# Optimization experiments

Hardware: AMD Instinct MI355X
Metric: run time of the kernel (lower is better)

The kernel has to match this reference:

```python
import jax, jax.numpy as jnp
import numpy as np

N_NODES = 100000
N_EDGES = 1600000
N_GRAPHS = 256
EPS = 1e-5  # GraphNorm / BatchNorm eps


def _seg_sum(x, seg, n):
    return jax.ops.segment_sum(x, seg, num_segments=n)


def setup_inputs() -> dict:
    key = jax.random.key(0)
    ks = jax.random.split(key, 24)
    f32 = jnp.float32

    def nrm(k, shape, s=0.05):
        return jax.random.normal(k, shape, f32) * s

    inp = {}
    inp["x"] = jax.random.normal(ks[0], (N_NODES, 64), f32)
    inp["edge_attr"] = jax.random.normal(ks[1], (N_EDGES, 8), f32)
    # edge_mlp: Linear(8,16) -> ReLU -> Linear(16,1); final bias +2 keeps degrees positive
    inp["em_w1"] = nrm(ks[2], (16, 8), 0.1); inp["em_b1"] = jnp.zeros((16,), f32)
    inp["em_w2"] = nrm(ks[3], (1, 16), 0.1); inp["em_b2"] = jnp.full((1,), 2.0, f32)
    # GCNConv weights stored (in, out); PyG GCNConv lin has no bias, separate bias after aggregation
    inp["conv_w0"] = nrm(ks[4], (64, 128)); inp["conv_b0"] = jnp.zeros((128,), f32)
    inp["conv_w1"] = nrm(ks[5], (128, 128)); inp["conv_b1"] = jnp.zeros((128,), f32)
    inp["conv_w2"] = nrm(ks[6], (128, 128)); inp["conv_b2"] = jnp.zeros((128,), f32)
    # GraphNorm params: weight=1, bias=0, mean_scale=1 (PyG init)
    for i in range(3):
        inp[f"gn_w{i}"] = jnp.ones((128,), f32)
        inp[f"gn_b{i}"] = jnp.zeros((128,), f32)
        inp[f"gn_ms{i}"] = jnp.ones((128,), f32)
    # MLP head (weights stored (in,out)); BatchNorm1d eval: running_mean=0, running_var=1
    inp["lin_w0"] = nrm(ks[7], (128, 256)); inp["lin_b0"] = jnp.zeros((256,), f32)
    inp["bn_g0"] = jnp.ones((256,), f32); inp["bn_b0"] = jnp.zeros((256,), f32)
    inp["lin_w1"] = nrm(ks[8], (256, 128)); inp["lin_b1"] = jnp.zeros((128,), f32)
    inp["bn_g1"] = jnp.ones((128,), f32); inp["bn_b1"] = jnp.zeros((128,), f32)
    inp["out_w"] = nrm(ks[9], (128, 1)); inp["out_b"] = jnp.zeros((1,), f32)
    inp["edge_index"] = jax.random.randint(ks[10], (2, N_EDGES), 0, N_NODES)
    inp["batch"] = jnp.sort(jax.random.randint(ks[11], (N_NODES,), 0, N_GRAPHS))
    return inp


def _gcn_conv(h, W, b, src, tgt, ew):
    # PyG GCNConv with edge_weight: add self-loops (weight 1), symmetric normalization
    hw = h @ W  # [N, out]
    deg = _seg_sum(ew, tgt, N_NODES) + 1.0  # in-degree incl. self-loop
    dinv = jnp.where(deg > 0, jax.lax.rsqrt(deg), 0.0)
    norm_e = dinv[src] * ew * dinv[tgt]  # [E]
    agg = _seg_sum(norm_e[:, None] * hw[src], tgt, N_NODES)
    agg = agg + (dinv * dinv)[:, None] * hw  # self-loop contribution
    return agg + b


def _graph_norm(h, batch, w, b, ms, cnt):
    mean = _seg_sum(h, batch, N_GRAPHS) / cnt[:, None]  # [G, C]
    sub = h - ms * mean[batch]
    var = _seg_sum(sub * sub, batch, N_GRAPHS) / cnt[:, None]
    return w * sub / jnp.sqrt(var + EPS)[batch] + b


def reference(x, edge_attr, em_w1, em_b1, em_w2, em_b2,
              conv_w0, conv_b0, conv_w1, conv_b1, conv_w2, conv_b2,
              gn_w0, gn_b0, gn_ms0, gn_w1, gn_b1, gn_ms1, gn_w2, gn_b2, gn_ms2,
              lin_w0, lin_b0, bn_g0, bn_b0, lin_w1, lin_b1, bn_g1, bn_b1,
              out_w, out_b, edge_index, batch):
    src, tgt = edge_index[0], edge_index[1]
    ew = (jax.nn.relu(edge_attr @ em_w1.T + em_b1) @ em_w2.T + em_b2).reshape(-1)  # [E]
    cnt = jnp.maximum(_seg_sum(jnp.ones((N_NODES,), x.dtype), batch, N_GRAPHS), 1.0)

    h = x
    layers = [(conv_w0, conv_b0, gn_w0, gn_b0, gn_ms0),
              (conv_w1, conv_b1, gn_w1, gn_b1, gn_ms1),
              (conv_w2, conv_b2, gn_w2, gn_b2, gn_ms2)]
    for W, b, gw, gb, gms in layers:
        h = _gcn_conv(h, W, b, src, tgt, ew)
        h = _graph_norm(h, batch, gw, gb, gms, cnt)
        h = jax.nn.relu(h)  # dropout is identity in eval mode

    pooled = _seg_sum(h, batch, N_GRAPHS) / cnt[:, None]  # global_mean_pool [G, 128]

    inv = 1.0 / jnp.sqrt(1.0 + EPS)  # BatchNorm1d eval: mean=0, var=1
    h = jax.nn.relu((pooled @ lin_w0 + lin_b0) * inv * bn_g0 + bn_b0)
    h = jax.nn.relu((h @ lin_w1 + lin_b1) * inv * bn_g1 + bn_b1)
    out = h @ out_w + out_b  # [G, 1]
    return (out, h)
```

## Files before the change

kernel.cpp:

```cpp
#include <hip/hip_runtime.h>

#define N_NODES 100000
#define N_EDGES 1600000
#define N_GRAPHS 256
#define EPS 1e-5f

#define SCAN_BLOCKS ((N_NODES + 255) / 256)

#define EB 6250
#define CB 3125
#define WB 128
#define W0B 32
#define PREP_BLOCKS (EB + CB + WB + W0B + 2)

typedef __attribute__((ext_vector_type(8))) short bfrag8;
typedef __attribute__((ext_vector_type(4))) float facc4;

__device__ __forceinline__ void fma4(float4& a, float s, const float4& w) {
  a.x += s * w.x; a.y += s * w.y; a.z += s * w.z; a.w += s * w.w;
}

__device__ __forceinline__ unsigned short f2bf(float f) {
  union { float f; unsigned u; } x;
  x.f = f;
  unsigned r = x.u + 0x7FFF + ((x.u >> 16) & 1);
  return (unsigned short)(r >> 16);
}
__device__ __forceinline__ unsigned packbf(float a, float b) {
  return (unsigned)f2bf(a) | ((unsigned)f2bf(b) << 16);
}
__device__ __forceinline__ float4 bf4(unsigned lo, unsigned hi) {
  union { unsigned u; float f; } a, b, c, d;
  a.u = lo << 16;
  b.u = lo & 0xFFFF0000u;
  c.u = hi << 16;
  d.u = hi & 0xFFFF0000u;
  return make_float4(a.f, b.f, c.f, d.f);
}
__device__ __forceinline__ float bfat(const unsigned* tb, int idx) {
  unsigned u = tb[idx >> 1];
  union { unsigned u; float f; } v;
  v.u = (idx & 1) ? (u & 0xFFFF0000u) : (u << 16);
  return v.f;
}

__global__ __launch_bounds__(256) void k_prep(
    const float* __restrict__ ea, const float* __restrict__ w1,
    const float* __restrict__ b1, const float* __restrict__ w2,
    const float* __restrict__ b2, const int* __restrict__ tgt,
    float* __restrict__ ew, int* __restrict__ rowcnt, int* __restrict__ rank,
    const float* __restrict__ x, unsigned* __restrict__ xb,
    const float* __restrict__ cw1, const float* __restrict__ cw2,
    unsigned short* __restrict__ wt1, unsigned short* __restrict__ wt2,
    const float* __restrict__ cw0, unsigned short* __restrict__ wt0,
    const int* __restrict__ batch, int* __restrict__ start) {
  __shared__ float W1[128], B1[16], W2[16];
  const int b = blockIdx.x;
  const int t = threadIdx.x;
  if (b < EB) {
    if (t < 128) W1[t] = w1[t];
    if (t < 16) { B1[t] = b1[t]; W2[t] = w2[t]; }
    __syncthreads();
    int e = b * 256 + t;
    if (e >= N_EDGES) return;
    const float4* ap = (const float4*)(ea + (size_t)e * 8);
    float4 a0 = ap[0], a1 = ap[1];
    float a[8] = {a0.x, a0.y, a0.z, a0.w, a1.x, a1.y, a1.z, a1.w};
    float out = b2[0];
#pragma unroll
    for (int i = 0; i < 16; ++i) {
      float h = B1[i];
#pragma unroll
      for (int j = 0; j < 8; ++j) h += a[j] * W1[i * 8 + j];
      out += fmaxf(h, 0.f) * W2[i];
    }
    ew[e] = out;
    rank[e] = atomicAdd(&rowcnt[tgt[e]], 1);
  } else if (b < EB + CB) {
    int i = (b - EB) * 256 + t;
    if (i >= N_NODES * 64 / 8) return;
    const float4* p = (const float4*)(x + (size_t)i * 8);
    float4 a = p[0], bb = p[1];
    uint4 o;
    o.x = packbf(a.x, a.y);
    o.y = packbf(a.z, a.w);
    o.z = packbf(bb.x, bb.y);
    o.w = packbf(bb.z, bb.w);
    ((uint4*)xb)[i] = o;
  } else if (b < EB + CB + WB) {
    int lb = b - EB - CB;
    int half = lb >> 6;
    int id = (lb & 63) * 256 + t;
    const float* w = half ? cw2 : cw1;
    unsigned short* o = half ? wt2 : wt1;
    int n = id >> 7, k = id & 127;
    o[n * 128 + k] = f2bf(w[k * 128 + n]);
  } else if (b < EB + CB + WB + W0B) {
    int id = (b - EB - CB - WB) * 256 + t;
    if (id >= 8192) return;
    int n = id >> 6, k = id & 63;
    wt0[n * 64 + k] = f2bf(cw0[k * 128 + n]);
  } else {
    int g = (b - EB - CB - WB - W0B) * 256 + t;
    if (g > N_GRAPHS) return;
    int lo = 0, hi = N_NODES;
    while (lo < hi) {
      int mid = (lo + hi) >> 1;
      if (batch[mid] < g) lo = mid + 1; else hi = mid;
    }
    start[g] = lo;
  }
}

__global__ __launch_bounds__(256) void k_scan1(const int* __restrict__ cnt,
                                               int* __restrict__ bsum) {
  int i = blockIdx.x * 256 + threadIdx.x;
  int v = (i < N_NODES) ? cnt[i] : 0;
#pragma unroll
  for (int off = 32; off; off >>= 1) v += __shfl_down(v, off);
  __shared__ int ws[4];
  if ((threadIdx.x & 63) == 0) ws[threadIdx.x >> 6] = v;
  __syncthreads();
  if (threadIdx.x == 0) bsum[blockIdx.x] = ws[0] + ws[1] + ws[2] + ws[3];
}

__global__ __launch_bounds__(512) void k_scan2(const int* __restrict__ bsum,
                                               int* __restrict__ boff) {
  __shared__ int s[512];
  int t = threadIdx.x;
  s[t] = (t < SCAN_BLOCKS) ? bsum[t] : 0;
  __syncthreads();
  for (int off = 1; off < 512; off <<= 1) {
    int u = (t >= off) ? s[t - off] : 0;
    __syncthreads();
    s[t] += u;
    __syncthreads();
  }
  boff[t] = (t == 0) ? 0 : s[t - 1];
}

__global__ __launch_bounds__(256) void k_scan3(const int* __restrict__ cnt,
                                               const int* __restrict__ boff,
                                               int* __restrict__ rowstart) {
  __shared__ int s[256];
  int t = threadIdx.x;
  int i = blockIdx.x * 256 + t;
  int v = (i < N_NODES) ? cnt[i] : 0;
  s[t] = v;
  __syncthreads();
  for (int off = 1; off < 256; off <<= 1) {
    int u = (t >= off) ? s[t - off] : 0;
    __syncthreads();
    s[t] += u;
    __syncthreads();
  }
  if (i < N_NODES) {
    int pre = boff[blockIdx.x] + s[t] - v;
    rowstart[i] = pre;
    if (i == N_NODES - 1) rowstart[N_NODES] = pre + v;
  }
}

__global__ __launch_bounds__(256) void k_fill(
    const int* __restrict__ src, const int* __restrict__ tgt,
    const float* __restrict__ ew, const int* __restrict__ rank,
    const int* __restrict__ rowstart, uint2* __restrict__ meta) {
  int e = blockIdx.x * 256 + threadIdx.x;
  if (e >= N_EDGES) return;
  int p = rowstart[tgt[e]] + rank[e];
  union { float f; unsigned u; } w;
  w.f = ew[e];
  meta[p] = make_uint2(w.u, (unsigned)src[e]);
}

__global__ __launch_bounds__(256) void k_deg(const uint2* __restrict__ meta,
                                             const int* __restrict__ rowstart,
                                             float* __restrict__ dinv) {
  int n = blockIdx.x * 256 + threadIdx.x;
  if (n >= N_NODES) return;
  int rs = rowstart[n], re = rowstart[n + 1];
  float d = 1.f;
  for (int j = rs; j < re; ++j) {
    union { unsigned u; float f; } w;
    w.u = meta[j].x;
    d += w.f;
  }
  dinv[n] = d > 0.f ? rsqrtf(d) : 0.f;
}

__global__ __launch_bounds__(256) void k_scale(uint2* __restrict__ meta,
                                               const int* __restrict__ rowstart,
                                               const float* __restrict__ dinv) {
  int n = blockIdx.x * 4 + (threadIdx.x >> 6);
  if (n >= N_NODES) return;
  int lane = threadIdx.x & 63;
  int rs = rowstart[n], re = rowstart[n + 1];
  float dv = dinv[n];
  for (int j = rs + lane; j < re; j += 64) {
    uint2 m = meta[j];
    union { unsigned u; float f; } w;
    w.u = m.x;
    w.f *= dinv[m.y] * dv;
    meta[j].x = w.u;
  }
}

__global__ __launch_bounds__(256) void k_gather64b(
    const unsigned* __restrict__ xb, const uint2* __restrict__ meta,
    const int* __restrict__ rowstart, const float* __restrict__ dinv,
    unsigned* __restrict__ aggxb) {
  const int t = threadIdx.x;
  const int n = blockIdx.x * 4 + (t >> 6);
  if (n >= N_NODES) return;
  const unsigned lane = t & 63;
  const unsigned q = lane >> 4;
  const unsigned cl = lane & 15;
  const int rs = rowstart[n], re = rowstart[n + 1];
  const uint2* x2 = (const uint2*)xb;
  float4 a0 = make_float4(0.f, 0.f, 0.f, 0.f);
  float4 a1 = make_float4(0.f, 0.f, 0.f, 0.f);
  int j = rs;
  for (; j + 8 <= re; j += 8) {
    uint2 m0 = meta[j + q], m1 = meta[j + 4 + q];
    union { unsigned u; float f; } w0, w1;
    w0.u = m0.x; w1.u = m1.x;
    uint2 v0 = x2[(m0.y << 4) + cl];
    uint2 v1 = x2[(m1.y << 4) + cl];
    fma4(a0, w0.f, bf4(v0.x, v0.y));
    fma4(a1, w1.f, bf4(v1.x, v1.y));
  }
  for (; j + 4 <= re; j += 4) {
    uint2 m0 = meta[j + q];
    union { unsigned u; float f; } w0;
    w0.u = m0.x;
    uint2 v0 = x2[(m0.y << 4) + cl];
    fma4(a0, w0.f, bf4(v0.x, v0.y));
  }
  if (j + (int)q < re) {
    uint2 m0 = meta[j + q];
    union { unsigned u; float f; } w0;
    w0.u = m0.x;
    uint2 v0 = x2[(m0.y << 4) + cl];
    fma4(a1, w0.f, bf4(v0.x, v0.y));
  }
  a0.x += a1.x; a0.y += a1.y; a0.z += a1.z; a0.w += a1.w;
#pragma unroll
  for (int m = 16; m <= 32; m <<= 1) {
    a0.x += __shfl_xor(a0.x, m);
    a0.y += __shfl_xor(a0.y, m);
    a0.z += __shfl_xor(a0.z, m);
    a0.w += __shfl_xor(a0.w, m);
  }
  if (q == 0) {
    float dv = dinv[n];
    uint2 hvb = x2[((unsigned)n << 4) + cl];
    float4 hv = bf4(hvb.x, hvb.y);
    uint2 o;
    o.x = packbf(a0.x + dv * dv * hv.x, a0.y + dv * dv * hv.y);
    o.y = packbf(a0.z + dv * dv * hv.z, a0.w + dv * dv * hv.w);
    *(uint2*)&aggxb[(size_t)n * 32 + cl * 2] = o;
  }
}

__global__ __launch_bounds__(256) void k_hw_mfma0(
    const unsigned short* __restrict__ aggxb,
    const unsigned short* __restrict__ wt0, const float* __restrict__ bias,
    unsigned short* __restrict__ h1b) {
  __shared__ unsigned short Asb[64][72];
  __shared__ unsigned short Wsb[128][72];
  const int t = threadIdx.x;
  const int base = blockIdx.x * 64;

  for (int i = t; i < 1024; i += 256) {
    int nr = i >> 3, k8 = (i & 7) * 8;
    *(uint4*)&Wsb[nr][k8] = *(const uint4*)&wt0[nr * 64 + k8];
  }
  {
    const int ln = t >> 2;
    const int kp = (t & 3) * 16;
    const int n = base + ln;
    if (n < N_NODES) {
      *(uint4*)&Asb[ln][kp] = *(const uint4*)&aggxb[(size_t)n * 64 + kp];
      *(uint4*)&Asb[ln][kp + 8] = *(const uint4*)&aggxb[(size_t)n * 64 + kp + 8];
    } else {
      uint4 z = make_uint4(0, 0, 0, 0);
      *(uint4*)&Asb[ln][kp] = z;
      *(uint4*)&Asb[ln][kp + 8] = z;
    }
  }
  __syncthreads();

  const int wv = t >> 6;
  const int lr = t & 15;
  const int lk = (t >> 4) & 3;
  const int m0 = wv * 16;

  bfrag8 af[2];
#pragma unroll
  for (int kc = 0; kc < 2; ++kc)
    af[kc] = *(const bfrag8*)&Asb[m0 + lr][kc * 32 + lk * 8];

#pragma unroll
  for (int nt = 0; nt < 8; ++nt) {
    facc4 c = {0.f, 0.f, 0.f, 0.f};
#pragma unroll
    for (int kc = 0; kc < 2; ++kc) {
      bfrag8 bf = *(const bfrag8*)&Wsb[nt * 16 + lr][kc * 32 + lk * 8];
      c = __builtin_amdgcn_mfma_f32_16x16x32_bf16(af[kc], bf, c, 0, 0, 0);
    }
    int col = nt * 16 + lr;
    float bv = bias[col];
#pragma unroll
    for (int r = 0; r < 4; ++r) {
      int n = base + m0 + lk * 4 + r;
      if (n < N_NODES) h1b[(size_t)n * 128 + col] = f2bf(c[r] + bv);
    }
  }
}

__global__ __launch_bounds__(256) void k_hw_mfma(
    const unsigned* __restrict__ hb, const unsigned short* __restrict__ wt,
    const int* __restrict__ batch, const float* __restrict__ An,
    const float* __restrict__ Bn, unsigned short* __restrict__ hwb) {
  __shared__ unsigned short Asb[64][136];
  __shared__ unsigned short Wsb[128][136];
  const int t = threadIdx.x;
  const int base = blockIdx.x * 64;

  for (int i = t; i < 2048; i += 256) {
    int nr = i >> 4, k8 = (i & 15) * 8;
    *(uint4*)&Wsb[nr][k8] = *(const uint4*)&wt[nr * 128 + k8];
  }
  {
    const int ln = t >> 2;
    const int cg = (t & 3) * 32;
    const int n = base + ln;
    if (n < N_NODES) {
      const int g = batch[n];
      const uint4* hp = (const uint4*)(hb + (size_t)n * 64);
      const float* Ap = An + (size_t)g * 128;
      const float* Bp = Bn + (size_t)g * 128;
#pragma unroll
      for (int qq = 0; qq < 4; ++qq) {
        int c = cg + qq * 8;
        uint4 v = hp[(t & 3) * 4 + qq];
        float4 lo = bf4(v.x, v.y);
        float4 hi = bf4(v.z, v.w);
        float4 Alo = *(const float4*)&Ap[c], Blo = *(const float4*)&Bp[c];
        float4 Ahi = *(const float4*)&Ap[c + 4], Bhi = *(const float4*)&Bp[c + 4];
        uint4 o;
        o.x = packbf(fmaxf(Alo.x * lo.x + Blo.x, 0.f),
                     fmaxf(Alo.y * lo.y + Blo.y, 0.f));
        o.y = packbf(fmaxf(Alo.z * lo.z + Blo.z, 0.f),
                     fmaxf(Alo.w * lo.w + Blo.w, 0.f));
        o.z = packbf(fmaxf(Ahi.x * hi.x + Bhi.x, 0.f),
                     fmaxf(Ahi.y * hi.y + Bhi.y, 0.f));
        o.w = packbf(fmaxf(Ahi.z * hi.z + Bhi.z, 0.f),
                     fmaxf(Ahi.w * hi.w + Bhi.w, 0.f));
        *(uint4*)&Asb[ln][c] = o;
      }
    } else {
      uint4 z = make_uint4(0, 0, 0, 0);
#pragma unroll
      for (int qq = 0; qq < 4; ++qq) *(uint4*)&Asb[ln][cg + qq * 8] = z;
    }
  }
  __syncthreads();

  const int wv = t >> 6;
  const int lr = t & 15;
  const int lk = (t >> 4) & 3;
  const int m0 = wv * 16;

  bfrag8 af[4];
#pragma unroll
  for (int kc = 0; kc < 4; ++kc)
    af[kc] = *(const bfrag8*)&Asb[m0 + lr][kc * 32 + lk * 8];

#pragma unroll
  for (int nt = 0; nt < 8; ++nt) {
    facc4 c = {0.f, 0.f, 0.f, 0.f};
#pragma unroll
    for (int kc = 0; kc < 4; ++kc) {
      bfrag8 bf = *(const bfrag8*)&Wsb[nt * 16 + lr][kc * 32 + lk * 8];
      c = __builtin_amdgcn_mfma_f32_16x16x32_bf16(af[kc], bf, c, 0, 0, 0);
    }
    int col = nt * 16 + lr;
#pragma unroll
    for (int r = 0; r < 4; ++r) {
      int n = base + m0 + lk * 4 + r;
      if (n < N_NODES) hwb[(size_t)n * 128 + col] = f2bf(c[r]);
    }
  }
}

__global__ __launch_bounds__(256) void k_gatherb(
    const unsigned* __restrict__ hwb, const uint2* __restrict__ meta,
    const int* __restrict__ rowstart, const float* __restrict__ dinv,
    const float* __restrict__ bias, unsigned* __restrict__ aggb) {
  const int t = threadIdx.x;
  const int n = blockIdx.x * 4 + (t >> 6);
  if (n >= N_NODES) return;
  const unsigned lane = t & 63;
  const unsigned q = lane >> 5;
  const unsigned cl = lane & 31;
  const int rs = rowstart[n], re = rowstart[n + 1];
  const uint2* hb = (const uint2*)hwb;
  float4 a0 = make_float4(0.f, 0.f, 0.f, 0.f);
  float4 a1 = make_float4(0.f, 0.f, 0.f, 0.f);
  float4 a2 = make_float4(0.f, 0.f, 0.f, 0.f);
  float4 a3 = make_float4(0.f, 0.f, 0.f, 0.f);
  int j = rs;
  for (; j + 8 <= re; j += 8) {
    uint2 m0 = meta[j + q], m1 = meta[j + 2 + q];
    uint2 m2 = meta[j + 4 + q], m3 = meta[j + 6 + q];
    union { unsigned u; float f; } w0, w1, w2, w3;
    w0.u = m0.x; w1.u = m1.x; w2.u = m2.x; w3.u = m3.x;
    uint2 v0 = hb[(m0.y << 5) + cl];
    uint2 v1 = hb[(m1.y << 5) + cl];
    uint2 v2 = hb[(m2.y << 5) + cl];
    uint2 v3 = hb[(m3.y << 5) + cl];
    fma4(a0, w0.f, bf4(v0.x, v0.y));
    fma4(a1, w1.f, bf4(v1.x, v1.y));
    fma4(a2, w2.f, bf4(v2.x, v2.y));
    fma4(a3, w3.f, bf4(v3.x, v3.y));
  }
  for (; j + 4 <= re; j += 4) {
    uint2 m0 = meta[j + q], m1 = meta[j + 2 + q];
    union { unsigned u; float f; } w0, w1;
    w0.u = m0.x; w1.u = m1.x;
    uint2 v0 = hb[(m0.y << 5) + cl];
    uint2 v1 = hb[(m1.y << 5) + cl];
    fma4(a0, w0.f, bf4(v0.x, v0.y));
    fma4(a1, w1.f, bf4(v1.x, v1.y));
  }
  for (; j + 2 <= re; j += 2) {
    uint2 m0 = meta[j + q];
    union { unsigned u; float f; } w0;
    w0.u = m0.x;
    uint2 v0 = hb[(m0.y << 5) + cl];
    fma4(a0, w0.f, bf4(v0.x, v0.y));
  }
  if (q == 0 && j < re) {
    uint2 m0 = meta[j];
    union { unsigned u; float f; } w0;
    w0.u = m0.x;
    uint2 v0 = hb[(m0.y << 5) + cl];
    fma4(a1, w0.f, bf4(v0.x, v0.y));
  }
  a0.x += a1.x + a2.x + a3.x;
  a0.y += a1.y + a2.y + a3.y;
  a0.z += a1.z + a2.z + a3.z;
  a0.w += a1.w + a2.w + a3.w;
  a0.x += __shfl_xor(a0.x, 32);
  a0.y += __shfl_xor(a0.y, 32);
  a0.z += __shfl_xor(a0.z, 32);
  a0.w += __shfl_xor(a0.w, 32);
  if (q == 0) {
    float dv = dinv[n];
    uint2 hvb = hb[((unsigned)n << 5) + cl];
    float4 hv = bf4(hvb.x, hvb.y);
    float4 bv = ((const float4*)bias)[cl];
    uint2 o;
    o.x = packbf(a0.x + dv * dv * hv.x + bv.x, a0.y + dv * dv * hv.y + bv.y);
    o.y = packbf(a0.z + dv * dv * hv.z + bv.z, a0.w + dv * dv * hv.w + bv.w);
    *(uint2*)&aggb[(size_t)n * 64 + cl * 2] = o;
  }
}

__global__ __launch_bounds__(512) void k_gstats(
    const unsigned* __restrict__ hb, const int* __restrict__ start,
    const float* __restrict__ gw, const float* __restrict__ gb,
    const float* __restrict__ gms, float* __restrict__ An,
    float* __restrict__ Bn) {
  int g = blockIdx.x;
  int s = start[g], e = start[g + 1];
  int t = threadIdx.x, p = t >> 7, c = t & 127;
  float sum = 0.f, sq = 0.f;
  for (int n = s + p; n < e; n += 4) {
    float v = bfat(hb + (size_t)n * 64, c);
    sum += v;
    sq += v * v;
  }
  __shared__ float S[4][128], Q[4][128];
  S[p][c] = sum;
  Q[p][c] = sq;
  __syncthreads();
  if (t < 128) {
    float cnt = (float)max(e - s, 1);
    float mean = (S[0][t] + S[1][t] + S[2][t] + S[3][t]) / cnt;
    float e2 = (Q[0][t] + Q[1][t] + Q[2][t] + Q[3][t]) / cnt;
    float ms = gms[t];
    float var = fmaxf(e2 - ms * (2.f - ms) * mean * mean, 0.f);
    float scale = gw[t] / sqrtf(var + EPS);
    An[(size_t)g * 128 + t] = scale;
    Bn[(size_t)g * 128 + t] = gb[t] - scale * ms * mean;
  }
}

__global__ __launch_bounds__(512) void k_pool(
    const unsigned* __restrict__ hb, const int* __restrict__ start,
    const float* __restrict__ An, const float* __restrict__ Bn,
    float* __restrict__ pooled) {
  int g = blockIdx.x;
  int s = start[g], e = start[g + 1];
  int t = threadIdx.x, p = t >> 7, c = t & 127;
  float A = An[(size_t)g * 128 + c], B = Bn[(size_t)g * 128 + c];
  float sum = 0.f;
  for (int n = s + p; n < e; n += 4)
    sum += fmaxf(A * bfat(hb + (size_t)n * 64, c) + B, 0.f);
  __shared__ float S[4][128];
  S[p][c] = sum;
  __syncthreads();
  if (t < 128) {
    float cnt = (float)max(e - s, 1);
    pooled[g * 128 + t] = (S[0][t] + S[1][t] + S[2][t] + S[3][t]) / cnt;
  }
}

__global__ __launch_bounds__(256) void k_head(
    const float* __restrict__ pooled, const float* __restrict__ w0,
    const float* __restrict__ b0, const float* __restrict__ g0,
    const float* __restrict__ bb0, const float* __restrict__ w1,
    const float* __restrict__ b1, const float* __restrict__ g1,
    const float* __restrict__ bb1, const float* __restrict__ ow,
    const float* __restrict__ ob, float* __restrict__ out) {
  __shared__ float p[128], h1[256], h2[128];
  int g = blockIdx.x, t = threadIdx.x;
  const float inv = 1.0f / sqrtf(1.0f + EPS);
  if (t < 128) p[t] = pooled[g * 128 + t];
  __syncthreads();
  {
    float acc = b0[t];
#pragma unroll 8
    for (int k = 0; k < 128; ++k) acc += p[k] * w0[k * 256 + t];
    h1[t] = fmaxf(acc * inv * g0[t] + bb0[t], 0.f);
  }
  __syncthreads();
  if (t < 128) {
    float acc = b1[t];
#pragma unroll 8
    for (int k = 0; k < 256; ++k) acc += h1[k] * w1[k * 128 + t];
    float v = fmaxf(acc * inv * g1[t] + bb1[t], 0.f);
    h2[t] = v;
    out[N_GRAPHS + g * 128 + t] = v;
  }
  __syncthreads();
  if (t < 64) {
    float v = h2[t] * ow[t] + h2[t + 64] * ow[t + 64];
#pragma unroll
    for (int off = 32; off; off >>= 1) v += __shfl_down(v, off);
    if (t == 0) out[g] = v + ob[0];
  }
}

extern "C" void kernel_launch(void* const* d_in, const int* in_sizes, int n_in,
                              void* d_out, int out_size, void* d_ws,
                              size_t ws_size, hipStream_t stream) {
  const float* x = (const float*)d_in[0];
  const float* edge_attr = (const float*)d_in[1];
  const float* em_w1 = (const float*)d_in[2];
  const float* em_b1 = (const float*)d_in[3];
  const float* em_w2 = (const float*)d_in[4];
  const float* em_b2 = (const float*)d_in[5];
  const float* conv_w[3] = {(const float*)d_in[6], (const float*)d_in[8],
                            (const float*)d_in[10]};
  const float* conv_b[3] = {(const float*)d_in[7], (const float*)d_in[9],
                            (const float*)d_in[11]};
  const float* gn_w[3] = {(const float*)d_in[12], (const float*)d_in[15],
                          (const float*)d_in[18]};
  const float* gn_b[3] = {(const float*)d_in[13], (const float*)d_in[16],
                          (const float*)d_in[19]};
  const float* gn_ms[3] = {(const float*)d_in[14], (const float*)d_in[17],
                           (const float*)d_in[20]};
  const float* lin_w0 = (const float*)d_in[21];
  const float* lin_b0 = (const float*)d_in[22];
  const float* bn_g0 = (const float*)d_in[23];
  const float* bn_b0 = (const float*)d_in[24];
  const float* lin_w1 = (const float*)d_in[25];
  const float* lin_b1 = (const float*)d_in[26];
  const float* bn_g1 = (const float*)d_in[27];
  const float* bn_b1 = (const float*)d_in[28];
  const float* out_w = (const float*)d_in[29];
  const float* out_b = (const float*)d_in[30];
  const int* edge_index = (const int*)d_in[31];
  const int* batch = (const int*)d_in[32];
  const int* src = edge_index;
  const int* tgt = edge_index + N_EDGES;

  char* w = (char*)d_ws;
  size_t off = 0;
  auto carve = [&](size_t bytes) {
    void* p = w + off;
    off = (off + bytes + 511) & ~(size_t)511;
    return p;
  };
  float* ew = (float*)carve((size_t)N_EDGES * 4);
  int* rank = (int*)carve((size_t)N_EDGES * 4);
  float* dinv = (float*)carve((size_t)N_NODES * 4);
  int* rowcnt = (int*)carve((size_t)N_NODES * 4);
  int* rowstart = (int*)carve((size_t)(N_NODES + 1) * 4);
  int* bsum = (int*)carve((size_t)SCAN_BLOCKS * 4);
  int* boff = (int*)carve((size_t)512 * 4);
  uint2* meta = (uint2*)carve((size_t)N_EDGES * 8);
  int* start = (int*)carve((N_GRAPHS + 1) * 4);
  float* AB = (float*)carve((size_t)6 * N_GRAPHS * 128 * 4);
  unsigned* xb = (unsigned*)carve((size_t)N_NODES * 64 * 2);
  unsigned* aggxb = (unsigned*)carve((size_t)N_NODES * 64 * 2);
  unsigned* h1b = (unsigned*)carve((size_t)N_NODES * 128 * 2);
  unsigned* hwb = (unsigned*)carve((size_t)N_NODES * 128 * 2);
  unsigned* agg1b = (unsigned*)carve((size_t)N_NODES * 128 * 2);
  unsigned* agg2b = (unsigned*)carve((size_t)N_NODES * 128 * 2);
  unsigned short* wt0 = (unsigned short*)carve((size_t)128 * 64 * 2);
  unsigned short* wt1 = (unsigned short*)carve((size_t)128 * 128 * 2);
  unsigned short* wt2 = (unsigned short*)carve((size_t)128 * 128 * 2);
  float* pooled = (float*)carve((size_t)N_GRAPHS * 128 * 4);

  float* A0 = AB, *B0 = AB + N_GRAPHS * 128;
  float* A1 = AB + 2 * N_GRAPHS * 128, *B1 = AB + 3 * N_GRAPHS * 128;
  float* A2 = AB + 4 * N_GRAPHS * 128, *B2 = AB + 5 * N_GRAPHS * 128;

  hipMemsetAsync(rowcnt, 0, (size_t)N_NODES * 4, stream);

  k_prep<<<PREP_BLOCKS, 256, 0, stream>>>(
      edge_attr, em_w1, em_b1, em_w2, em_b2, tgt, ew, rowcnt, rank, x, xb,
      conv_w[1], conv_w[2], wt1, wt2, conv_w[0], wt0, batch, start);
  k_scan1<<<SCAN_BLOCKS, 256, 0, stream>>>(rowcnt, bsum);
  k_scan2<<<1, 512, 0, stream>>>(bsum, boff);
  k_scan3<<<SCAN_BLOCKS, 256, 0, stream>>>(rowcnt, boff, rowstart);
  k_fill<<<(N_EDGES + 255) / 256, 256, 0, stream>>>(src, tgt, ew, rank,
                                                    rowstart, meta);
  k_deg<<<(N_NODES + 255) / 256, 256, 0, stream>>>(meta, rowstart, dinv);
  k_scale<<<(N_NODES + 3) / 4, 256, 0, stream>>>(meta, rowstart, dinv);

  const int ggrid = (N_NODES + 3) / 4;
  const int hwgrid = (N_NODES + 63) / 64;

  k_gather64b<<<ggrid, 256, 0, stream>>>(xb, meta, rowstart, dinv, aggxb);
  k_hw_mfma0<<<hwgrid, 256, 0, stream>>>((unsigned short*)aggxb, wt0,
                                         conv_b[0], (unsigned short*)h1b);
  k_gstats<<<N_GRAPHS, 512, 0, stream>>>(h1b, start, gn_w[0], gn_b[0],
                                         gn_ms[0], A0, B0);
  k_hw_mfma<<<hwgrid, 256, 0, stream>>>(h1b, wt1, batch, A0, B0,
                                        (unsigned short*)hwb);
  k_gatherb<<<ggrid, 256, 0, stream>>>(hwb, meta, rowstart, dinv, conv_b[1],
                                       agg1b);
  k_gstats<<<N_GRAPHS, 512, 0, stream>>>(agg1b, start, gn_w[1], gn_b[1],
                                         gn_ms[1], A1, B1);
  k_hw_mfma<<<hwgrid, 256, 0, stream>>>(agg1b, wt2, batch, A1, B1,
                                        (unsigned short*)hwb);
  k_gatherb<<<ggrid, 256, 0, stream>>>(hwb, meta, rowstart, dinv, conv_b[2],
                                       agg2b);
  k_gstats<<<N_GRAPHS, 512, 0, stream>>>(agg2b, start, gn_w[2], gn_b[2],
                                         gn_ms[2], A2, B2);

  k_pool<<<N_GRAPHS, 512, 0, stream>>>(agg2b, start, A2, B2, pooled);
  k_head<<<N_GRAPHS, 256, 0, stream>>>(pooled, lin_w0, lin_b0, bn_g0, bn_b0,
                                       lin_w1, lin_b1, bn_g1, bn_b1, out_w,
                                       out_b, (float*)d_out);
}
```

Before: 520.3 us.

## Fold source-side degree normalization into features and widen gather loads

Symmetric GCN normalization is refactored: the source-side dinv factor is folded into the feature rows (at x->bf16 conversion and in the MFMA epilogue), and the target-side factor is applied once after aggregation, so edge weights no longer need a separate per-edge rescale pass. The deg and scale kernels are merged into one wave-per-node kernel that also does the x conversion, removing a pass over meta. The gather kernels switch to 16-byte loads with fewer lanes per row. Rounding changes slightly because dinv is applied before the bf16 cast.

Measured after the change: 525.5 us. Within noise of the previous version (+1.0%).

```diff
diff --git a/kernel.cpp b/kernel.cpp
--- a/kernel.cpp
+++ b/kernel.cpp
@@ -8,10 +8,9 @@
 #define SCAN_BLOCKS ((N_NODES + 255) / 256)
 
 #define EB 6250
-#define CB 3125
 #define WB 128
 #define W0B 32
-#define PREP_BLOCKS (EB + CB + WB + W0B + 2)
+#define PREP_BLOCKS (EB + WB + W0B + 2)
 
 typedef __attribute__((ext_vector_type(8))) short bfrag8;
 typedef __attribute__((ext_vector_type(4))) float facc4;
@@ -49,7 +48,6 @@
     const float* __restrict__ b1, const float* __restrict__ w2,
     const float* __restrict__ b2, const int* __restrict__ tgt,
     float* __restrict__ ew, int* __restrict__ rowcnt, int* __restrict__ rank,
-    const float* __restrict__ x, unsigned* __restrict__ xb,
     const float* __restrict__ cw1, const float* __restrict__ cw2,
     unsigned short* __restrict__ wt1, unsigned short* __restrict__ wt2,
     const float* __restrict__ cw0, unsigned short* __restrict__ wt0,
@@ -76,32 +74,21 @@
     }
     ew[e] = out;
     rank[e] = atomicAdd(&rowcnt[tgt[e]], 1);
-  } else if (b < EB + CB) {
-    int i = (b - EB) * 256 + t;
-    if (i >= N_NODES * 64 / 8) return;
-    const float4* p = (const float4*)(x + (size_t)i * 8);
-    float4 a = p[0], bb = p[1];
-    uint4 o;
-    o.x = packbf(a.x, a.y);
-    o.y = packbf(a.z, a.w);
-    o.z = packbf(bb.x, bb.y);
-    o.w = packbf(bb.z, bb.w);
-    ((uint4*)xb)[i] = o;
-  } else if (b < EB + CB + WB) {
-    int lb = b - EB - CB;
+  } else if (b < EB + WB) {
+    int lb = b - EB;
     int half = lb >> 6;
     int id = (lb & 63) * 256 + t;
     const float* w = half ? cw2 : cw1;
     unsigned short* o = half ? wt2 : wt1;
     int n = id >> 7, k = id & 127;
     o[n * 128 + k] = f2bf(w[k * 128 + n]);
-  } else if (b < EB + CB + WB + W0B) {
-    int id = (b - EB - CB - WB) * 256 + t;
+  } else if (b < EB + WB + W0B) {
+    int id = (b - EB - WB) * 256 + t;
     if (id >= 8192) return;
     int n = id >> 6, k = id & 63;
     wt0[n * 64 + k] = f2bf(cw0[k * 128 + n]);
   } else {
-    int g = (b - EB - CB - WB - W0B) * 256 + t;
+    int g = (b - EB - WB - W0B) * 256 + t;
     if (g > N_GRAPHS) return;
     int lo = 0, hi = N_NODES;
     while (lo < hi) {
@@ -173,35 +160,28 @@
   meta[p] = make_uint2(w.u, (unsigned)src[e]);
 }
 
-__global__ __launch_bounds__(256) void k_deg(const uint2* __restrict__ meta,
-                                             const int* __restrict__ rowstart,
-                                             float* __restrict__ dinv) {
-  int n = blockIdx.x * 256 + threadIdx.x;
+__global__ __launch_bounds__(256) void k_degcvt(
+    const uint2* __restrict__ meta, const int* __restrict__ rowstart,
+    const float* __restrict__ x, float* __restrict__ dinv,
+    unsigned* __restrict__ xb) {
+  const int n = blockIdx.x * 4 + (threadIdx.x >> 6);
   if (n >= N_NODES) return;
-  int rs = rowstart[n], re = rowstart[n + 1];
-  float d = 1.f;
-  for (int j = rs; j < re; ++j) {
+  const int lane = threadIdx.x & 63;
+  const int rs = rowstart[n], re = rowstart[n + 1];
+  float s = 0.f;
+  for (int j = rs + lane; j < re; j += 64) {
     union { unsigned u; float f; } w;
     w.u = meta[j].x;
-    d += w.f;
-  }
-  dinv[n] = d > 0.f ? rsqrtf(d) : 0.f;
-}
-
-__global__ __launch_bounds__(256) void k_scale(uint2* __restrict__ meta,
-                                               const int* __restrict__ rowstart,
-                                               const float* __restrict__ dinv) {
-  int n = blockIdx.x * 4 + (threadIdx.x >> 6);
-  if (n >= N_NODES) return;
-  int lane = threadIdx.x & 63;
-  int rs = rowstart[n], re = rowstart[n + 1];
-  float dv = dinv[n];
-  for (int j = rs + lane; j < re; j += 64) {
-    uint2 m = meta[j];
-    union { unsigned u; float f; } w;
-    w.u = m.x;
-    w.f *= dinv[m.y] * dv;
-    meta[j].x = w.u;
+    s += w.f;
+  }
+#pragma unroll
+  for (int m = 1; m < 64; m <<= 1) s += __shfl_xor(s, m);
+  float d = 1.f + s;
+  float dv = d > 0.f ? rsqrtf(d) : 0.f;
+  if (lane == 0) dinv[n] = dv;
+  if (lane < 32) {
+    float2 v = ((const float2*)x)[(size_t)n * 32 + lane];
+    xb[((unsigned)n << 5) + lane] = packbf(dv * v.x, dv * v.y);
   }
 }
 
@@ -213,52 +193,63 @@
   const int n = blockIdx.x * 4 + (t >> 6);
   if (n >= N_NODES) return;
   const unsigned lane = t & 63;
-  const unsigned q = lane >> 4;
-  const unsigned cl = lane & 15;
+  const unsigned q = lane >> 3;
+  const unsigned cl = lane & 7;
   const int rs = rowstart[n], re = rowstart[n + 1];
-  const uint2* x2 = (const uint2*)xb;
-  float4 a0 = make_float4(0.f, 0.f, 0.f, 0.f);
-  float4 a1 = make_float4(0.f, 0.f, 0.f, 0.f);
+  const uint4* x4 = (const uint4*)xb;
+  float4 lo0 = make_float4(0.f, 0.f, 0.f, 0.f), hi0 = lo0;
+  float4 lo1 = lo0, hi1 = lo0;
   int j = rs;
-  for (; j + 8 <= re; j += 8) {
-    uint2 m0 = meta[j + q], m1 = meta[j + 4 + q];
+  for (; j + 16 <= re; j += 16) {
+    uint2 m0 = meta[j + q], m1 = meta[j + 8 + q];
     union { unsigned u; float f; } w0, w1;
     w0.u = m0.x; w1.u = m1.x;
-    uint2 v0 = x2[(m0.y << 4) + cl];
-    uint2 v1 = x2[(m1.y << 4) + cl];
-    fma4(a0, w0.f, bf4(v0.x, v0.y));
-    fma4(a1, w1.f, bf4(v1.x, v1.y));
-  }
-  for (; j + 4 <= re; j += 4) {
+    uint4 v0 = x4[(m0.y << 3) + cl];
+    uint4 v1 = x4[(m1.y << 3) + cl];
+    fma4(lo0, w0.f, bf4(v0.x, v0.y));
+    fma4(hi0, w0.f, bf4(v0.z, v0.w));
+    fma4(lo1, w1.f, bf4(v1.x, v1.y));
+    fma4(hi1, w1.f, bf4(v1.z, v1.w));
+  }
+  for (; j + 8 <= re; j += 8) {
     uint2 m0 = meta[j + q];
     union { unsigned u; float f; } w0;
     w0.u = m0.x;
-    uint2 v0 = x2[(m0.y << 4) + cl];
-    fma4(a0, w0.f, bf4(v0.x, v0.y));
+    uint4 v0 = x4[(m0.y << 3) + cl];
+    fma4(lo0, w0.f, bf4(v0.x, v0.y));
+    fma4(hi0, w0.f, bf4(v0.z, v0.w));
   }
   if (j + (int)q < re) {
     uint2 m0 = meta[j + q];
     union { unsigned u; float f; } w0;
     w0.u = m0.x;
-    uint2 v0 = x2[(m0.y << 4) + cl];
-    fma4(a1, w0.f, bf4(v0.x, v0.y));
-  }
-  a0.x += a1.x; a0.y += a1.y; a0.z += a1.z; a0.w += a1.w;
-#pragma unroll
-  for (int m = 16; m <= 32; m <<= 1) {
-    a0.x += __shfl_xor(a0.x, m);
-    a0.y += __shfl_xor(a0.y, m);
-    a0.z += __shfl_xor(a0.z, m);
-    a0.w += __shfl_xor(a0.w, m);
+    uint4 v0 = x4[(m0.y << 3) + cl];
+    fma4(lo1, w0.f, bf4(v0.x, v0.y));
+    fma4(hi1, w0.f, bf4(v0.z, v0.w));
+  }
+  lo0.x += lo1.x; lo0.y += lo1.y; lo0.z += lo1.z; lo0.w += lo1.w;
+  hi0.x += hi1.x; hi0.y += hi1.y; hi0.z += hi1.z; hi0.w += hi1.w;
+#pragma unroll
+  for (int m = 8; m <= 32; m <<= 1) {
+    lo0.x += __shfl_xor(lo0.x, m);
+    lo0.y += __shfl_xor(lo0.y, m);
+    lo0.z += __shfl_xor(lo0.z, m);
+    lo0.w += __shfl_xor(lo0.w, m);
+    hi0.x += __shfl_xor(hi0.x, m);
+    hi0.y += __shfl_xor(hi0.y, m);
+    hi0.z += __shfl_xor(hi0.z, m);
+    hi0.w += __shfl_xor(hi0.w, m);
   }
   if (q == 0) {
     float dv = dinv[n];
-    uint2 hvb = x2[((unsigned)n << 4) + cl];
-    float4 hv = bf4(hvb.x, hvb.y);
-    uint2 o;
-    o.x = packbf(a0.x + dv * dv * hv.x, a0.y + dv * dv * hv.y);
-    o.y = packbf(a0.z + dv * dv * hv.z, a0.w + dv * dv * hv.w);
-    *(uint2*)&aggxb[(size_t)n * 32 + cl * 2] = o;
+    uint4 sv = x4[((unsigned)n << 3) + cl];
+    float4 slo = bf4(sv.x, sv.y), shi = bf4(sv.z, sv.w);
+    uint4 o;
+    o.x = packbf(dv * (lo0.x + slo.x), dv * (lo0.y + slo.y));
+    o.y = packbf(dv * (lo0.z + slo.z), dv * (lo0.w + slo.w));
+    o.z = packbf(dv * (hi0.x + shi.x), dv * (hi0.y + shi.y));
+    o.w = packbf(dv * (hi0.z + shi.z), dv * (hi0.w + shi.w));
+    ((uint4*)aggxb)[((unsigned)n << 3) + cl] = o;
   }
 }
 
@@ -321,7 +312,8 @@
 __global__ __launch_bounds__(256) void k_hw_mfma(
     const unsigned* __restrict__ hb, const unsigned short* __restrict__ wt,
     const int* __restrict__ batch, const float* __restrict__ An,
-    const float* __restrict__ Bn, unsigned short* __restrict__ hwb) {
+    const float* __restrict__ Bn, const float* __restrict__ dinv,
+    unsigned short* __restrict__ hwb) {
   __shared__ unsigned short Asb[64][136];
   __shared__ unsigned short Wsb[128][136];
   const int t = threadIdx.x;
@@ -377,6 +369,13 @@
   for (int kc = 0; kc < 4; ++kc)
     af[kc] = *(const bfrag8*)&Asb[m0 + lr][kc * 32 + lk * 8];
 
+  float dv[4];
+#pragma unroll
+  for (int r = 0; r < 4; ++r) {
+    int n = base + m0 + lk * 4 + r;
+    dv[r] = (n < N_NODES) ? dinv[n] : 0.f;
+  }
+
 #pragma unroll
   for (int nt = 0; nt < 8; ++nt) {
     facc4 c = {0.f, 0.f, 0.f, 0.f};
@@ -389,7 +388,7 @@
 #pragma unroll
     for (int r = 0; r < 4; ++r) {
       int n = base + m0 + lk * 4 + r;
-      if (n < N_NODES) hwb[(size_t)n * 128 + col] = f2bf(c[r]);
+      if (n < N_NODES) hwb[(size_t)n * 128 + col] = f2bf(dv[r] * c[r]);
     }
   }
 }
@@ -402,69 +401,65 @@
   const int n = blockIdx.x * 4 + (t >> 6);
   if (n >= N_NODES) return;
   const unsigned lane = t & 63;
-  const unsigned q = lane >> 5;
-  const unsigned cl = lane & 31;
+  const unsigned q = lane >> 4;
+  const unsigned cl = lane & 15;
   const int rs = rowstart[n], re = rowstart[n + 1];
-  const uint2* hb = (const uint2*)hwb;
-  float4 a0 = make_float4(0.f, 0.f, 0.f, 0.f);
-  float4 a1 = make_float4(0.f, 0.f, 0.f, 0.f);
-  float4 a2 = make_float4(0.f, 0.f, 0.f, 0.f);
-  float4 a3 = make_float4(0.f, 0.f, 0.f, 0.f);
+  const uint4* hb4 = (const uint4*)hwb;
+  float4 lo0 = make_float4(0.f, 0.f, 0.f, 0.f), hi0 = lo0;
+  float4 lo1 = lo0, hi1 = lo0;
   int j = rs;
   for (; j + 8 <= re; j += 8) {
-    uint2 m0 = meta[j + q], m1 = meta[j + 2 + q];
-    uint2 m2 = meta[j + 4 + q], m3 = meta[j + 6 + q];
-    union { unsigned u; float f; } w0, w1, w2, w3;
-    w0.u = m0.x; w1.u = m1.x; w2.u = m2.x; w3.u = m3.x;
-    uint2 v0 = hb[(m0.y << 5) + cl];
-    uint2 v1 = hb[(m1.y << 5) + cl];
-    uint2 v2 = hb[(m2.y << 5) + cl];
-    uint2 v3 = hb[(m3.y << 5) + cl];
-    fma4(a0, w0.f, bf4(v0.x, v0.y));
-    fma4(a1, w1.f, bf4(v1.x, v1.y));
-    fma4(a2, w2.f, bf4(v2.x, v2.y));
-    fma4(a3, w3.f, bf4(v3.x, v3.y));
-  }
-  for (; j + 4 <= re; j += 4) {
-    uint2 m0 = meta[j + q], m1 = meta[j + 2 + q];
+    uint2 m0 = meta[j + q], m1 = meta[j + 4 + q];
     union { unsigned u; float f; } w0, w1;
     w0.u = m0.x; w1.u = m1.x;
-    uint2 v0 = hb[(m0.y << 5) + cl];
-    uint2 v1 = hb[(m1.y << 5) + cl];
-    fma4(a0, w0.f, bf4(v0.x, v0.y));
-    fma4(a1, w1.f, bf4(v1.x, v1.y));
-  }
-  for (; j + 2 <= re; j += 2) {
+    uint4 v0 = hb4[(m0.y << 4) + cl];
+    uint4 v1 = hb4[(m1.y << 4) + cl];
+    fma4(lo0, w0.f, bf4(v0.x, v0.y));
+    fma4(hi0, w0.f, bf4(v0.z, v0.w));
+    fma4(lo1, w1.f, bf4(v1.x, v1.y));
+    fma4(hi1, w1.f, bf4(v1.z, v1.w));
+  }
+  for (; j + 4 <= re; j += 4) {
     uint2 m0 = meta[j + q];
     union { unsigned u; float f; } w0;
     w0.u = m0.x;
-    uint2 v0 = hb[(m0.y << 5) + cl];
-    fma4(a0, w0.f, bf4(v0.x, v0.y));
-  }
-  if (q == 0 && j < re) {
-    uint2 m0 = meta[j];
+    uint4 v0 = hb4[(m0.y << 4) + cl];
+    fma4(lo0, w0.f, bf4(v0.x, v0.y));
+    fma4(hi0, w0.f, bf4(v0.z, v0.w));
+  }
+  if (j + (int)q < re) {
+    uint2 m0 = meta[j + q];
     union { unsigned u; float f; } w0;
     w0.u = m0.x;
-    uint2 v0 = hb[(m0.y << 5) + cl];
-    fma4(a1, w0.f, bf4(v0.x, v0.y));
-  }
-  a0.x += a1.x + a2.x + a3.x;
-  a0.y += a1.y + a2.y + a3.y;
-  a0.z += a1.z + a2.z + a3.z;
-  a0.w += a1.w + a2.w + a3.w;
-  a0.x += __shfl_xor(a0.x, 32);
-  a0.y += __shfl_xor(a0.y, 32);
-  a0.z += __shfl_xor(a0.z, 32);
-  a0.w += __shfl_xor(a0.w, 32);
+    uint4 v0 = hb4[(m0.y << 4) + cl];
+    fma4(lo1, w0.f, bf4(v0.x, v0.y));
+    fma4(hi1, w0.f, bf4(v0.z, v0.w));
+  }
+  lo0.x += lo1.x; lo0.y += lo1.y; lo0.z += lo1.z; lo0.w += lo1.w;
+  hi0.x += hi1.x; hi0.y += hi1.y; hi0.z += hi1.z; hi0.w += hi1.w;
+#pragma unroll
+  for (int m = 16; m <= 32; m <<= 1) {
+    lo0.x += __shfl_xor(lo0.x, m);
+    lo0.y += __shfl_xor(lo0.y, m);
+    lo0.z += __shfl_xor(lo0.z, m);
+    lo0.w += __shfl_xor(lo0.w, m);
+    hi0.x += __shfl_xor(hi0.x, m);
+    hi0.y += __shfl_xor(hi0.y, m);
+    hi0.z += __shfl_xor(hi0.z, m);
+    hi0.w += __shfl_xor(hi0.w, m);
+  }
   if (q == 0) {
     float dv = dinv[n];
-    uint2 hvb = hb[((unsigned)n << 5) + cl];
-    float4 hv = bf4(hvb.x, hvb.y);
-    float4 bv = ((const float4*)bias)[cl];
-    uint2 o;
-    o.x = packbf(a0.x + dv * dv * hv.x + bv.x, a0.y + dv * dv * hv.y + bv.y);
-    o.y = packbf(a0.z + dv * dv * hv.z + bv.z, a0.w + dv * dv * hv.w + bv.w);
-    *(uint2*)&aggb[(size_t)n * 64 + cl * 2] = o;
+    uint4 sv = hb4[((unsigned)n << 4) + cl];
+    float4 slo = bf4(sv.x, sv.y), shi = bf4(sv.z, sv.w);
+    float4 blo = *(const float4*)&bias[cl * 8];
+    float4 bhi = *(const float4*)&bias[cl * 8 + 4];
+    uint4 o;
+    o.x = packbf(dv * (lo0.x + slo.x) + blo.x, dv * (lo0.y + slo.y) + blo.y);
+    o.y = packbf(dv * (lo0.z + slo.z) + blo.z, dv * (lo0.w + slo.w) + blo.w);
+    o.z = packbf(dv * (hi0.x + shi.x) + bhi.x, dv * (hi0.y + shi.y) + bhi.y);
+    o.w = packbf(dv * (hi0.z + shi.z) + bhi.z, dv * (hi0.w + shi.w) + bhi.w);
+    ((uint4*)aggb)[((unsigned)n << 4) + cl] = o;
   }
 }
 
@@ -623,31 +618,31 @@
   hipMemsetAsync(rowcnt, 0, (size_t)N_NODES * 4, stream);
 
   k_prep<<<PREP_BLOCKS, 256, 0, stream>>>(
-      edge_attr, em_w1, em_b1, em_w2, em_b2, tgt, ew, rowcnt, rank, x, xb,
+      edge_attr, em_w1, em_b1, em_w2, em_b2, tgt, ew, rowcnt, rank,
       conv_w[1], conv_w[2], wt1, wt2, conv_w[0], wt0, batch, start);
   k_scan1<<<SCAN_BLOCKS, 256, 0, stream>>>(rowcnt, bsum);
   k_scan2<<<1, 512, 0, stream>>>(bsum, boff);
   k_scan3<<<SCAN_BLOCKS, 256, 0, stream>>>(rowcnt, boff, rowstart);
   k_fill<<<(N_EDGES + 255) / 256, 256, 0, stream>>>(src, tgt, ew, rank,
                                                     rowstart, meta);
-  k_deg<<<(N_NODES + 255) / 256, 256, 0, stream>>>(meta, rowstart, dinv);
-  k_scale<<<(N_NODES + 3) / 4, 256, 0, stream>>>(meta, rowstart, dinv);
 
   const int ggrid = (N_NODES + 3) / 4;
   const int hwgrid = (N_NODES + 63) / 64;
+
+  k_degcvt<<<ggrid, 256, 0, stream>>>(meta, rowstart, x, dinv, xb);
 
   k_gather64b<<<ggrid, 256, 0, stream>>>(xb, meta, rowstart, dinv, aggxb);
   k_hw_mfma0<<<hwgrid, 256, 0, stream>>>((unsigned short*)aggxb, wt0,
                                          conv_b[0], (unsigned short*)h1b);
   k_gstats<<<N_GRAPHS, 512, 0, stream>>>(h1b, start, gn_w[0], gn_b[0],
                                          gn_ms[0], A0, B0);
-  k_hw_mfma<<<hwgrid, 256, 0, stream>>>(h1b, wt1, batch, A0, B0,
+  k_hw_mfma<<<hwgrid, 256, 0, stream>>>(h1b, wt1, batch, A0, B0, dinv,
                                         (unsigned short*)hwb);
   k_gatherb<<<ggrid, 256, 0, stream>>>(hwb, meta, rowstart, dinv, conv_b[1],
                                        agg1b);
   k_gstats<<<N_GRAPHS, 512, 0, stream>>>(agg1b, start, gn_w[1], gn_b[1],
                                          gn_ms[1], A1, B1);
-  k_hw_mfma<<<hwgrid, 256, 0, stream>>>(agg1b, wt2, batch, A1, B1,
+  k_hw_mfma<<<hwgrid, 256, 0, stream>>>(agg1b, wt2, batch, A1, B1, dinv,
                                         (unsigned short*)hwb);
   k_gatherb<<<ggrid, 256, 0, stream>>>(hwb, meta, rowstart, dinv, conv_b[2],
                                        agg2b);
```
